# Optimization experiments

Hardware: AMD Instinct MI355X
Metric: run time of the kernel (lower is better)

## Reference

```python
import jax, jax.numpy as jnp
import numpy as np

DIM = 1024
NUM_HEADS = 16
HEAD_DIM = DIM // NUM_HEADS
EPS = 1e-5


def setup_inputs() -> dict:
    key = jax.random.key(0)
    ks = jax.random.split(key, 5)
    B, N = 2, 2048
    x = jax.random.normal(ks[0], (B, N, DIM), dtype=jnp.float32)
    # nn.Linear(dim, 3*dim): weight [3*dim, dim], bias [3*dim]
    w_qkv = jax.random.normal(ks[1], (3 * DIM, DIM), dtype=jnp.float32) * (DIM ** -0.5)
    b_qkv = jnp.zeros((3 * DIM,), dtype=jnp.float32)
    # qk-norm LayerNorm(head_dim) affine params
    q_gamma = jnp.ones((HEAD_DIM,), dtype=jnp.float32)
    q_beta = jnp.zeros((HEAD_DIM,), dtype=jnp.float32)
    k_gamma = jnp.ones((HEAD_DIM,), dtype=jnp.float32)
    k_beta = jnp.zeros((HEAD_DIM,), dtype=jnp.float32)
    # output projection nn.Linear(dim, dim)
    w_proj = jax.random.normal(ks[2], (DIM, DIM), dtype=jnp.float32) * (DIM ** -0.5)
    b_proj = jnp.zeros((DIM,), dtype=jnp.float32)
    return {
        "x": x,
        "w_qkv": w_qkv, "b_qkv": b_qkv,
        "q_gamma": q_gamma, "q_beta": q_beta,
        "k_gamma": k_gamma, "k_beta": k_beta,
        "w_proj": w_proj, "b_proj": b_proj,
    }


def _layernorm(t, gamma, beta):
    # LayerNorm over last dim (head_dim)
    mu = jnp.mean(t, axis=-1, keepdims=True)
    var = jnp.mean(jnp.square(t - mu), axis=-1, keepdims=True)
    return (t - mu) * jax.lax.rsqrt(var + EPS) * gamma + beta


def reference(x, w_qkv, b_qkv, q_gamma, q_beta, k_gamma, k_beta, w_proj, b_proj):
    B, N, C = x.shape
    H, D = NUM_HEADS, HEAD_DIM
    scale = D ** -0.5
    # QKV projection: [B,N,3C] -> [3,B,H,N,D]
    qkv = x @ w_qkv.T + b_qkv
    qkv = qkv.reshape(B, N, 3, H, D).transpose(2, 0, 3, 1, 4)
    q, k, v = qkv[0], qkv[1], qkv[2]
    # per-head qk-norm
    q = _layernorm(q, q_gamma, q_beta)
    k = _layernorm(k, k_gamma, k_beta)
    # scaled dot-product attention
    scores = jnp.einsum("bhqd,bhkd->bhqk", q, k) * scale
    attn = jax.nn.softmax(scores, axis=-1)
    out = jnp.einsum("bhqk,bhkd->bhqd", attn, v)  # [B,H,N,D]
    out = out.transpose(0, 2, 1, 3).reshape(B, N, C)
    # output projection
    return out @ w_proj.T + b_proj
```

## Files before the change

kernel.cpp:

```cpp
#include <hip/hip_runtime.h>

typedef _Float16 half8 __attribute__((ext_vector_type(8)));
typedef _Float16 half4 __attribute__((ext_vector_type(4)));
typedef float f32x4 __attribute__((ext_vector_type(4)));
typedef float f32x16 __attribute__((ext_vector_type(16)));
typedef unsigned int uint;
typedef uint uint4v __attribute__((ext_vector_type(4)));

#define MFMA16(a, b, c) __builtin_amdgcn_mfma_f32_16x16x32_f16((a), (b), (c), 0, 0, 0)
#define MFMA32(a, b, c) __builtin_amdgcn_mfma_f32_32x32x16_f16((a), (b), (c), 0, 0, 0)

#define GLOAD16(g, l)                                            \
    __builtin_amdgcn_global_load_lds(                            \
        (const __attribute__((address_space(1))) void*)(g),      \
        (__attribute__((address_space(3))) void*)(l), 16, 0, 0)


__global__ __launch_bounds__(256) void cvt_f32_f16(const float* __restrict__ in,
                                                   _Float16* __restrict__ out, int n8) {
    int i = blockIdx.x * 256 + threadIdx.x;
    if (i >= n8) return;
    const float4* p = reinterpret_cast<const float4*>(in) + 2 * (size_t)i;
    float4 a = p[0], b = p[1];
    half8 o;
    o[0] = (_Float16)a.x; o[1] = (_Float16)a.y; o[2] = (_Float16)a.z; o[3] = (_Float16)a.w;
    o[4] = (_Float16)b.x; o[5] = (_Float16)b.y; o[6] = (_Float16)b.z; o[7] = (_Float16)b.w;
    reinterpret_cast<half8*>(out)[i] = o;
}

template <int EPI>
__global__ __launch_bounds__(256) void gemm_nt(const _Float16* __restrict__ A,
                                               const _Float16* __restrict__ W,
                                               const float* __restrict__ bias,
                                               void* __restrict__ Cout, int K) {
    __shared__ __align__(16) _Float16 Al[128 * 64];
    __shared__ __align__(16) _Float16 Wl[128 * 64];
    const int tid = threadIdx.x, l = tid & 63, w = tid >> 6;
    const int bm = blockIdx.x * 128, bn = blockIdx.y * 128;
    const int wr = (w >> 1) * 64, wc = (w & 1) * 64;
    const int srow = l >> 3;
    const int schunk = (l & 7) ^ srow;

    f32x4 acc[4][4] = {};
    const _Float16* Ag = A + (size_t)(bm + 32 * w + srow) * K + 8 * schunk;
    const _Float16* Wg = W + (size_t)(bn + 32 * w + srow) * K + 8 * schunk;
    const int rswz = (l & 7) << 3;

    for (int kt = 0; kt < K; kt += 64) {
        __syncthreads();
#pragma unroll
        for (int t = 0; t < 4; t++) {
            GLOAD16(Ag + (size_t)(8 * t) * K + kt, &Al[(32 * w + 8 * t) * 64]);
            GLOAD16(Wg + (size_t)(8 * t) * K + kt, &Wl[(32 * w + 8 * t) * 64]);
        }
        __syncthreads();
#pragma unroll
        for (int ks = 0; ks < 2; ks++) {
            const int koff = (ks * 32 + (l >> 4) * 8) ^ rswz;
            half8 af[4], wf[4];
#pragma unroll
            for (int t = 0; t < 4; t++) {
                af[t] = *(const half8*)&Al[(wr + t * 16 + (l & 15)) * 64 + koff];
                wf[t] = *(const half8*)&Wl[(wc + t * 16 + (l & 15)) * 64 + koff];
            }
#pragma unroll
            for (int mt = 0; mt < 4; mt++)
#pragma unroll
                for (int nt = 0; nt < 4; nt++)
                    acc[mt][nt] = MFMA16(af[mt], wf[nt], acc[mt][nt]);
        }
    }
#pragma unroll
    for (int mt = 0; mt < 4; mt++)
#pragma unroll
        for (int nt = 0; nt < 4; nt++)
#pragma unroll
            for (int r = 0; r < 4; r++) {
                int m = bm + wr + mt * 16 + (l >> 4) * 4 + r;
                int n = bn + wc + nt * 16 + (l & 15);
                float v = acc[mt][nt][r] + bias[n];
                if (EPI == 0) {
                    int s = n >> 10, h = (n >> 6) & 15, d = n & 63;
                    int b = m >> 11, nn = m & 2047;
                    ((_Float16*)Cout)[(size_t)((((s * 2 + b) * 16 + h) * 2048 + nn) << 6) + d] =
                        (_Float16)v;
                } else {
                    ((float*)Cout)[(size_t)m * 1024 + n] = v;
                }
            }
}

__global__ __launch_bounds__(256) void ln_qk(_Float16* __restrict__ qkv,
                                             const float* __restrict__ qg,
                                             const float* __restrict__ qb,
                                             const float* __restrict__ kg,
                                             const float* __restrict__ kb) {
    const int l = threadIdx.x & 63, w = threadIdx.x >> 6;
    const int rid = blockIdx.x * 4 + w;
    const int s = rid >> 16;
    _Float16* base = qkv + (size_t)s * 4194304 + (size_t)(rid & 65535) * 64;
    float x = (float)base[l];
    float sm = x, s2 = x * x;
#pragma unroll
    for (int off = 1; off < 64; off <<= 1) {
        sm += __shfl_xor(sm, off);
        s2 += __shfl_xor(s2, off);
    }
    float mean = sm * (1.f / 64.f);
    float var = s2 * (1.f / 64.f) - mean * mean;
    float rs = rsqrtf(var + 1e-5f);
    float g = s ? kg[l] : qg[l];
    float be = s ? kb[l] : qb[l];
    base[l] = (_Float16)((x - mean) * rs * g + be);
}

__global__ __launch_bounds__(256) void attn_kernel(const _Float16* __restrict__ qkv,
                                                   _Float16* __restrict__ out) {
    const int tid = threadIdx.x;
    const int l = tid & 63, w = tid >> 6;
    const int l31 = l & 31, hi = l >> 5;
    const int head = blockIdx.x >> 4, qt = blockIdx.x & 15;
    const int b = head >> 4, h = head & 15;
    const size_t hstride = (size_t)2048 * 64;
    const _Float16* Q = qkv + (size_t)((0 + b) * 16 + h) * hstride;
    const _Float16* Kp = qkv + (size_t)((2 + b) * 16 + h) * hstride;
    const _Float16* Vp = qkv + (size_t)((4 + b) * 16 + h) * hstride;

    __shared__ __align__(16) _Float16 Kl[2][64 * 64];
    __shared__ __align__(16) _Float16 Vt[2][64 * 64];

    const int r0q = qt * 128 + w * 32;
    half8 qf[4];
    {
        const _Float16* Qrow = Q + (size_t)(r0q + l31) * 64 + 8 * hi;
#pragma unroll
        for (int dk = 0; dk < 4; dk++) {
            half8 v = *(const half8*)&Qrow[16 * dk];
#pragma unroll
            for (int i = 0; i < 8; i++) v[i] = v[i] * (_Float16)0.125f;
            qf[dk] = v;
        }
    }

    const int srow = l >> 3, sch = l & 7;
    auto stageK = [&](int it, _Float16* dst) {
#pragma unroll
        for (int t = 0; t < 2; t++) {
            int r0 = 16 * w + 8 * t;
            const _Float16* g = Kp + (size_t)(it * 64 + r0 + srow) * 64 + 8 * (sch ^ srow);
            GLOAD16(g, &dst[r0 * 64]);
        }
    };
    auto loadV = [&](int it, half8& v0, half8& v1) {
        const _Float16* g = Vp + (size_t)(it * 64 + 16 * w + srow) * 64 + 8 * sch;
        v0 = *(const half8*)g;
        v1 = *(const half8*)(g + 8 * 64);
    };
    auto scatterV = [&](half8 v0, half8 v1, _Float16* dst) {
        const int j0 = 16 * w + srow;
        const int d0 = 8 * sch;
#pragma unroll
        for (int i = 0; i < 8; i++) {
            const int sw = (i ^ sch) << 3;
            dst[(d0 + i) * 64 + (j0 ^ sw)] = v0[i];
            dst[(d0 + i) * 64 + ((j0 + 8) ^ sw)] = v1[i];
        }
    };

    float mrun = -1e30f, lrun = 0.f;
    f32x16 o0 = {}, o1 = {};

    half8 va, vb;
    stageK(0, Kl[0]);
    loadV(0, va, vb);
    scatterV(va, vb, Vt[0]);
    __syncthreads();

    const int kswz = (l31 & 7) << 3;
    const int vswz0 = ((l31 & 7) ^ (l31 >> 3)) << 3;
    const int vswz1 = vswz0 ^ (4 << 3);

    for (int it = 0; it < 32; ++it) {
        const int cur = it & 1;
        const _Float16* Kc = Kl[cur];
        const _Float16* Vc = Vt[cur];
        if (it + 1 < 32) {
            stageK(it + 1, Kl[cur ^ 1]);
            loadV(it + 1, va, vb);
        }
        f32x16 st0 = {}, st1 = {};
#pragma unroll
        for (int dk = 0; dk < 4; dk++) {
            const int colr = 16 * dk + 8 * hi;
            half8 kf0 = *(const half8*)&Kc[l31 * 64 + (colr ^ kswz)];
            half8 kf1 = *(const half8*)&Kc[(32 + l31) * 64 + (colr ^ kswz)];
            st0 = MFMA32(kf0, qf[dk], st0);
            st1 = MFMA32(kf1, qf[dk], st1);
        }
        float mh = st0[0];
#pragma unroll
        for (int r = 1; r < 16; r++) mh = fmaxf(mh, st0[r]);
#pragma unroll
        for (int r = 0; r < 16; r++) mh = fmaxf(mh, st1[r]);
        mh = fmaxf(mh, __shfl_xor(mh, 32));
        const float mnew = fmaxf(mrun, mh);
        const float alpha = __expf(mrun - mnew);
        mrun = mnew;
        float lh = 0.f;
#pragma unroll
        for (int r = 0; r < 16; r++) { st0[r] = __expf(st0[r] - mnew); lh += st0[r]; }
#pragma unroll
        for (int r = 0; r < 16; r++) { st1[r] = __expf(st1[r] - mnew); lh += st1[r]; }
        lh += __shfl_xor(lh, 32);
        lrun = lrun * alpha + lh;
#pragma unroll
        for (int r = 0; r < 16; r++) { o0[r] *= alpha; o1[r] *= alpha; }

#define PV_CHUNK(stv, c)                                                                   \
        {                                                                                  \
            uint pk0 = __builtin_bit_cast(uint, __builtin_amdgcn_cvt_pkrtz(stv[(c & 1) * 8 + 0], stv[(c & 1) * 8 + 1])); \
            uint pk1 = __builtin_bit_cast(uint, __builtin_amdgcn_cvt_pkrtz(stv[(c & 1) * 8 + 2], stv[(c & 1) * 8 + 3])); \
            uint pk2 = __builtin_bit_cast(uint, __builtin_amdgcn_cvt_pkrtz(stv[(c & 1) * 8 + 4], stv[(c & 1) * 8 + 5])); \
            uint pk3 = __builtin_bit_cast(uint, __builtin_amdgcn_cvt_pkrtz(stv[(c & 1) * 8 + 6], stv[(c & 1) * 8 + 7])); \
            uint sa = __shfl_xor(pk0, 32), sb = __shfl_xor(pk1, 32);                       \
            uint sc = __shfl_xor(pk2, 32), sd = __shfl_xor(pk3, 32);                       \
            uint4v fu = {hi ? sc : pk0, hi ? sd : pk1, hi ? pk2 : sa, hi ? pk3 : sb};      \
            half8 pfrag = __builtin_bit_cast(half8, fu);                                   \
            const int colc = 16 * (c) + 8 * hi;                                            \
            half8 vf0 = *(const half8*)&Vc[l31 * 64 + (colc ^ vswz0)];                     \
            half8 vf1 = *(const half8*)&Vc[(32 + l31) * 64 + (colc ^ vswz1)];              \
            o0 = MFMA32(vf0, pfrag, o0);                                                   \
            o1 = MFMA32(vf1, pfrag, o1);                                                   \
        }
        PV_CHUNK(st0, 0)
        PV_CHUNK(st0, 1)
        PV_CHUNK(st1, 2)
        PV_CHUNK(st1, 3)
#undef PV_CHUNK

        if (it + 1 < 32) scatterV(va, vb, Vt[cur ^ 1]);
        __syncthreads();
    }

    const float inv = __builtin_amdgcn_rcpf(lrun);
    const int tok = r0q + l31;
    _Float16* orow = out + (size_t)(b * 2048 + tok) * 1024 + h * 64;
#pragma unroll
    for (int g = 0; g < 4; g++) {
        half4 h4a, h4b;
#pragma unroll
        for (int j = 0; j < 4; j++) {
            h4a[j] = (_Float16)(o0[4 * g + j] * inv);
            h4b[j] = (_Float16)(o1[4 * g + j] * inv);
        }
        *(half4*)&orow[8 * g + 4 * hi] = h4a;
        *(half4*)&orow[32 + 8 * g + 4 * hi] = h4b;
    }
}

extern "C" void kernel_launch(void* const* d_in, const int* in_sizes, int n_in,
                              void* d_out, int out_size, void* d_ws, size_t ws_size,
                              hipStream_t stream) {
    const float* x = (const float*)d_in[0];
    const float* w_qkv = (const float*)d_in[1];
    const float* b_qkv = (const float*)d_in[2];
    const float* q_gamma = (const float*)d_in[3];
    const float* q_beta = (const float*)d_in[4];
    const float* k_gamma = (const float*)d_in[5];
    const float* k_beta = (const float*)d_in[6];
    const float* w_proj = (const float*)d_in[7];
    const float* b_proj = (const float*)d_in[8];

    char* ws = (char*)d_ws;
    _Float16* xh = (_Float16*)(ws + 0);
    _Float16* wqkvh = (_Float16*)(ws + 8388608);
    _Float16* wprojh = (_Float16*)(ws + 14680064);
    _Float16* qkvh = (_Float16*)(ws + 16777216);
    _Float16* attnh = (_Float16*)(ws + 41943040);

    cvt_f32_f16<<<2048, 256, 0, stream>>>(x, xh, 524288);
    cvt_f32_f16<<<1536, 256, 0, stream>>>(w_qkv, wqkvh, 393216);
    cvt_f32_f16<<<512, 256, 0, stream>>>(w_proj, wprojh, 131072);

    gemm_nt<0><<<dim3(32, 24), 256, 0, stream>>>(xh, wqkvh, b_qkv, (void*)qkvh, 1024);

    ln_qk<<<32768, 256, 0, stream>>>(qkvh, q_gamma, q_beta, k_gamma, k_beta);

    attn_kernel<<<512, 256, 0, stream>>>(qkvh, attnh);

    gemm_nt<1><<<dim3(32, 8), 256, 0, stream>>>(attnh, wprojh, b_proj, d_out, 1024);
}
```

Measured before the change: 252.9 us.

## Fuse qk-norm into QKV GEMM epilogue and drop online softmax max tracking

Merges the three f32-to-f16 conversion launches into one kernel. Folds the per-head q/k LayerNorm into the QKV GEMM epilogue, reducing across 16 lanes, and pre-scales q by scale*log2(e). That removes the separate ln_qk pass over the qkv buffer. The attention kernel drops the running max and rescaling and uses exp2 directly, relying on normalized q/k keeping scores bounded. Also adds XCD-aware block remapping for the GEMM and attention grids and s_setprio around MFMA bursts.

```diff
diff --git a/kernel.cpp b/kernel.cpp
--- a/kernel.cpp
+++ b/kernel.cpp
@@ -16,27 +16,43 @@
         (__attribute__((address_space(3))) void*)(l), 16, 0, 0)
 
 
-__global__ __launch_bounds__(256) void cvt_f32_f16(const float* __restrict__ in,
-                                                   _Float16* __restrict__ out, int n8) {
+__global__ __launch_bounds__(256) void cvt_all(const float* __restrict__ x,
+                                               const float* __restrict__ wq,
+                                               const float* __restrict__ wp,
+                                               _Float16* __restrict__ xh,
+                                               _Float16* __restrict__ wqh,
+                                               _Float16* __restrict__ wph) {
     int i = blockIdx.x * 256 + threadIdx.x;
-    if (i >= n8) return;
-    const float4* p = reinterpret_cast<const float4*>(in) + 2 * (size_t)i;
+    const float* src;
+    _Float16* dst;
+    int off;
+    if (i < 524288) { src = x; dst = xh; off = i; }
+    else if (i < 917504) { src = wq; dst = wqh; off = i - 524288; }
+    else { src = wp; dst = wph; off = i - 917504; }
+    const float4* p = reinterpret_cast<const float4*>(src) + 2 * (size_t)off;
     float4 a = p[0], b = p[1];
     half8 o;
     o[0] = (_Float16)a.x; o[1] = (_Float16)a.y; o[2] = (_Float16)a.z; o[3] = (_Float16)a.w;
     o[4] = (_Float16)b.x; o[5] = (_Float16)b.y; o[6] = (_Float16)b.z; o[7] = (_Float16)b.w;
-    reinterpret_cast<half8*>(out)[i] = o;
+    reinterpret_cast<half8*>(dst)[off] = o;
 }
 
 template <int EPI>
 __global__ __launch_bounds__(256) void gemm_nt(const _Float16* __restrict__ A,
                                                const _Float16* __restrict__ W,
                                                const float* __restrict__ bias,
-                                               void* __restrict__ Cout, int K) {
+                                               void* __restrict__ Cout, int K,
+                                               const float* __restrict__ qg,
+                                               const float* __restrict__ qb,
+                                               const float* __restrict__ kg,
+                                               const float* __restrict__ kb) {
     __shared__ __align__(16) _Float16 Al[128 * 64];
     __shared__ __align__(16) _Float16 Wl[128 * 64];
     const int tid = threadIdx.x, l = tid & 63, w = tid >> 6;
-    const int bm = blockIdx.x * 128, bn = blockIdx.y * 128;
+    const int lin = blockIdx.x + (blockIdx.y << 5);
+    const int nwg = gridDim.x * gridDim.y;
+    const int wg = (lin & 7) * (nwg >> 3) + (lin >> 3);
+    const int bm = (wg & 31) * 128, bn = (wg >> 5) * 128;
     const int wr = (w >> 1) * 64, wc = (w & 1) * 64;
     const int srow = l >> 3;
     const int schunk = (l & 7) ^ srow;
@@ -63,55 +79,80 @@
                 af[t] = *(const half8*)&Al[(wr + t * 16 + (l & 15)) * 64 + koff];
                 wf[t] = *(const half8*)&Wl[(wc + t * 16 + (l & 15)) * 64 + koff];
             }
+            __builtin_amdgcn_s_setprio(1);
 #pragma unroll
             for (int mt = 0; mt < 4; mt++)
 #pragma unroll
                 for (int nt = 0; nt < 4; nt++)
                     acc[mt][nt] = MFMA16(af[mt], wf[nt], acc[mt][nt]);
-        }
-    }
-#pragma unroll
-    for (int mt = 0; mt < 4; mt++)
-#pragma unroll
-        for (int nt = 0; nt < 4; nt++)
+            __builtin_amdgcn_s_setprio(0);
+        }
+    }
+
+    if (EPI == 0) {
+        const int ncol = bn + wc;
+        const int s = ncol >> 10;
+        const int hh = (ncol >> 6) & 15;
+        const float* gam = (s == 0) ? qg : kg;
+        const float* bet = (s == 0) ? qb : kb;
+        float ga[4], be[4];
+        if (s < 2) {
+#pragma unroll
+            for (int nt = 0; nt < 4; nt++) {
+                int d = nt * 16 + (l & 15);
+                ga[nt] = gam[d];
+                be[nt] = bet[d];
+            }
+        }
+        const float cs = (s == 0) ? 0.18033688f : 1.f;
+#pragma unroll
+        for (int mt = 0; mt < 4; mt++)
 #pragma unroll
             for (int r = 0; r < 4; r++) {
+                float v[4];
+                float sm = 0.f, s2 = 0.f;
+#pragma unroll
+                for (int nt = 0; nt < 4; nt++) {
+                    v[nt] = acc[mt][nt][r] + bias[ncol + nt * 16 + (l & 15)];
+                    sm += v[nt];
+                    s2 += v[nt] * v[nt];
+                }
                 int m = bm + wr + mt * 16 + (l >> 4) * 4 + r;
-                int n = bn + wc + nt * 16 + (l & 15);
-                float v = acc[mt][nt][r] + bias[n];
-                if (EPI == 0) {
-                    int s = n >> 10, h = (n >> 6) & 15, d = n & 63;
-                    int b = m >> 11, nn = m & 2047;
-                    ((_Float16*)Cout)[(size_t)((((s * 2 + b) * 16 + h) * 2048 + nn) << 6) + d] =
-                        (_Float16)v;
+                int b = m >> 11, nn = m & 2047;
+                _Float16* dst = (_Float16*)Cout +
+                    (size_t)((((s * 2 + b) * 16 + hh) * 2048 + nn) << 6);
+                if (s < 2) {
+#pragma unroll
+                    for (int off = 1; off < 16; off <<= 1) {
+                        sm += __shfl_xor(sm, off);
+                        s2 += __shfl_xor(s2, off);
+                    }
+                    float mean = sm * (1.f / 64.f);
+                    float var = s2 * (1.f / 64.f) - mean * mean;
+                    float rs = rsqrtf(var + 1e-5f) * cs;
+#pragma unroll
+                    for (int nt = 0; nt < 4; nt++) {
+                        int d = nt * 16 + (l & 15);
+                        dst[d] = (_Float16)((v[nt] - mean) * rs * ga[nt] + be[nt] * cs);
+                    }
                 } else {
-                    ((float*)Cout)[(size_t)m * 1024 + n] = v;
+#pragma unroll
+                    for (int nt = 0; nt < 4; nt++)
+                        dst[nt * 16 + (l & 15)] = (_Float16)v[nt];
                 }
             }
-}
-
-__global__ __launch_bounds__(256) void ln_qk(_Float16* __restrict__ qkv,
-                                             const float* __restrict__ qg,
-                                             const float* __restrict__ qb,
-                                             const float* __restrict__ kg,
-                                             const float* __restrict__ kb) {
-    const int l = threadIdx.x & 63, w = threadIdx.x >> 6;
-    const int rid = blockIdx.x * 4 + w;
-    const int s = rid >> 16;
-    _Float16* base = qkv + (size_t)s * 4194304 + (size_t)(rid & 65535) * 64;
-    float x = (float)base[l];
-    float sm = x, s2 = x * x;
-#pragma unroll
-    for (int off = 1; off < 64; off <<= 1) {
-        sm += __shfl_xor(sm, off);
-        s2 += __shfl_xor(s2, off);
-    }
-    float mean = sm * (1.f / 64.f);
-    float var = s2 * (1.f / 64.f) - mean * mean;
-    float rs = rsqrtf(var + 1e-5f);
-    float g = s ? kg[l] : qg[l];
-    float be = s ? kb[l] : qb[l];
-    base[l] = (_Float16)((x - mean) * rs * g + be);
+    } else {
+#pragma unroll
+        for (int mt = 0; mt < 4; mt++)
+#pragma unroll
+            for (int nt = 0; nt < 4; nt++)
+#pragma unroll
+                for (int r = 0; r < 4; r++) {
+                    int m = bm + wr + mt * 16 + (l >> 4) * 4 + r;
+                    int n = bn + wc + nt * 16 + (l & 15);
+                    ((float*)Cout)[(size_t)m * 1024 + n] = acc[mt][nt][r] + bias[n];
+                }
+    }
 }
 
 __global__ __launch_bounds__(256) void attn_kernel(const _Float16* __restrict__ qkv,
@@ -119,7 +160,9 @@
     const int tid = threadIdx.x;
     const int l = tid & 63, w = tid >> 6;
     const int l31 = l & 31, hi = l >> 5;
-    const int head = blockIdx.x >> 4, qt = blockIdx.x & 15;
+    const int bid = blockIdx.x;
+    const int wg = (bid & 7) * 64 + (bid >> 3);
+    const int head = wg >> 4, qt = wg & 15;
     const int b = head >> 4, h = head & 15;
     const size_t hstride = (size_t)2048 * 64;
     const _Float16* Q = qkv + (size_t)((0 + b) * 16 + h) * hstride;
@@ -134,12 +177,7 @@
     {
         const _Float16* Qrow = Q + (size_t)(r0q + l31) * 64 + 8 * hi;
 #pragma unroll
-        for (int dk = 0; dk < 4; dk++) {
-            half8 v = *(const half8*)&Qrow[16 * dk];
-#pragma unroll
-            for (int i = 0; i < 8; i++) v[i] = v[i] * (_Float16)0.125f;
-            qf[dk] = v;
-        }
+        for (int dk = 0; dk < 4; dk++) qf[dk] = *(const half8*)&Qrow[16 * dk];
     }
 
     const int srow = l >> 3, sch = l & 7;
@@ -167,7 +205,7 @@
         }
     };
 
-    float mrun = -1e30f, lrun = 0.f;
+    float lrun = 0.f;
     f32x16 o0 = {}, o1 = {};
 
     half8 va, vb;
@@ -194,27 +232,17 @@
             const int colr = 16 * dk + 8 * hi;
             half8 kf0 = *(const half8*)&Kc[l31 * 64 + (colr ^ kswz)];
             half8 kf1 = *(const half8*)&Kc[(32 + l31) * 64 + (colr ^ kswz)];
+            __builtin_amdgcn_s_setprio(1);
             st0 = MFMA32(kf0, qf[dk], st0);
             st1 = MFMA32(kf1, qf[dk], st1);
-        }
-        float mh = st0[0];
-#pragma unroll
-        for (int r = 1; r < 16; r++) mh = fmaxf(mh, st0[r]);
-#pragma unroll
-        for (int r = 0; r < 16; r++) mh = fmaxf(mh, st1[r]);
-        mh = fmaxf(mh, __shfl_xor(mh, 32));
-        const float mnew = fmaxf(mrun, mh);
-        const float alpha = __expf(mrun - mnew);
-        mrun = mnew;
+            __builtin_amdgcn_s_setprio(0);
+        }
         float lh = 0.f;
 #pragma unroll
-        for (int r = 0; r < 16; r++) { st0[r] = __expf(st0[r] - mnew); lh += st0[r]; }
-#pragma unroll
-        for (int r = 0; r < 16; r++) { st1[r] = __expf(st1[r] - mnew); lh += st1[r]; }
-        lh += __shfl_xor(lh, 32);
-        lrun = lrun * alpha + lh;
-#pragma unroll
-        for (int r = 0; r < 16; r++) { o0[r] *= alpha; o1[r] *= alpha; }
+        for (int r = 0; r < 16; r++) { st0[r] = exp2f(st0[r]); lh += st0[r]; }
+#pragma unroll
+        for (int r = 0; r < 16; r++) { st1[r] = exp2f(st1[r]); lh += st1[r]; }
+        lrun += lh;
 
 #define PV_CHUNK(stv, c)                                                                   \
         {                                                                                  \
@@ -229,8 +257,10 @@
             const int colc = 16 * (c) + 8 * hi;                                            \
             half8 vf0 = *(const half8*)&Vc[l31 * 64 + (colc ^ vswz0)];                     \
             half8 vf1 = *(const half8*)&Vc[(32 + l31) * 64 + (colc ^ vswz1)];              \
+            __builtin_amdgcn_s_setprio(1);                                                 \
             o0 = MFMA32(vf0, pfrag, o0);                                                   \
             o1 = MFMA32(vf1, pfrag, o1);                                                   \
+            __builtin_amdgcn_s_setprio(0);                                                 \
         }
         PV_CHUNK(st0, 0)
         PV_CHUNK(st0, 1)
@@ -242,6 +272,7 @@
         __syncthreads();
     }
 
+    lrun += __shfl_xor(lrun, 32);
     const float inv = __builtin_amdgcn_rcpf(lrun);
     const int tok = r0q + l31;
     _Float16* orow = out + (size_t)(b * 2048 + tok) * 1024 + h * 64;
@@ -278,15 +309,13 @@
     _Float16* qkvh = (_Float16*)(ws + 16777216);
     _Float16* attnh = (_Float16*)(ws + 41943040);
 
-    cvt_f32_f16<<<2048, 256, 0, stream>>>(x, xh, 524288);
-    cvt_f32_f16<<<1536, 256, 0, stream>>>(w_qkv, wqkvh, 393216);
-    cvt_f32_f16<<<512, 256, 0, stream>>>(w_proj, wprojh, 131072);
-
-    gemm_nt<0><<<dim3(32, 24), 256, 0, stream>>>(xh, wqkvh, b_qkv, (void*)qkvh, 1024);
-
-    ln_qk<<<32768, 256, 0, stream>>>(qkvh, q_gamma, q_beta, k_gamma, k_beta);
+    cvt_all<<<4096, 256, 0, stream>>>(x, w_qkv, w_proj, xh, wqkvh, wprojh);
+
+    gemm_nt<0><<<dim3(32, 24), 256, 0, stream>>>(xh, wqkvh, b_qkv, (void*)qkvh, 1024,
+                                                 q_gamma, q_beta, k_gamma, k_beta);
 
     attn_kernel<<<512, 256, 0, stream>>>(qkvh, attnh);
 
-    gemm_nt<1><<<dim3(32, 8), 256, 0, stream>>>(attnh, wprojh, b_proj, d_out, 1024);
+    gemm_nt<1><<<dim3(32, 8), 256, 0, stream>>>(attnh, wprojh, b_proj, d_out, 1024,
+                                                nullptr, nullptr, nullptr, nullptr);
 }
```

Result: faster. 223.3 us (-11.7%).
